# Optimization experiments

Hardware: AMD Instinct MI355X
Metric: run time of the kernel (lower is better)

## Reference

```python
import jax, jax.numpy as jnp
import numpy as np

B, S, D = 4, 512, 2048
N_HEADS, N_KV, HEAD_DIM = 16, 4, 128
N_REP = N_HEADS // N_KV
FFN = 5632
E, TOPK, R = 8, 2, 16
LORA_SCALE = 32.0 / R  # alpha / r
EPS = 1e-5


def setup_inputs() -> dict:
    key = jax.random.key(0)
    ks = jax.random.split(key, 32)

    def p(k, shape, s=0.02):
        return jax.random.normal(k, shape, jnp.float32) * s

    data = jax.random.normal(ks[0], (B, S, D), jnp.float32)
    # causal additive mask [1,1,S,S]
    causal = jnp.tril(jnp.ones((S, S), jnp.bool_))
    mask = jnp.where(causal, 0.0, -1e9).astype(jnp.float32)[None, None]
    # rotary angles (llama interleaved pairing), half head_dim
    inv_freq = 1.0 / (10000.0 ** (np.arange(0, HEAD_DIM, 2, dtype=np.float32) / HEAD_DIM))
    angles = jnp.asarray(np.arange(S, dtype=np.float32)[:, None] * inv_freq[None, :])
    rope_cos = jnp.cos(angles)  # [S, HEAD_DIM//2]
    rope_sin = jnp.sin(angles)

    inp = dict(
        data=data, mask=mask, rope_cos=rope_cos, rope_sin=rope_sin,
        att_norm_w=jnp.ones((D,), jnp.float32),
        ffn_norm_w=jnp.ones((D,), jnp.float32),
        wq=p(ks[1], (D, D)), wk=p(ks[2], (N_KV * HEAD_DIM, D)),
        wv=p(ks[3], (N_KV * HEAD_DIM, D)), wo=p(ks[4], (D, D)),
        lqA=p(ks[5], (R, D)), lqB=p(ks[6], (D, R)),
        lkA=p(ks[7], (R, D)), lkB=p(ks[8], (N_KV * HEAD_DIM, R)),
        lvA=p(ks[9], (R, D)), lvB=p(ks[10], (N_KV * HEAD_DIM, R)),
        loA=p(ks[11], (R, D)), loB=p(ks[12], (D, R)),
        w1=p(ks[13], (FFN, D)), w2=p(ks[14], (D, FFN)), w3=p(ks[15], (FFN, D)),
        gate_w=p(ks[16], (E, D)),
        eA1=p(ks[17], (E, R, D)), eB1=p(ks[18], (E, FFN, R)),
        eA2=p(ks[19], (E, R, FFN)), eB2=p(ks[20], (E, D, R)),
        eA3=p(ks[21], (E, R, D)), eB3=p(ks[22], (E, FFN, R)),
    )
    return inp


def rmsnorm(x, w):
    return x * jax.lax.rsqrt(jnp.mean(x * x, axis=-1, keepdims=True) + EPS) * w


def lora_linear(x, W, A, Bm):
    # torch Linear weight is [out, in]; lora: x @ A^T @ B^T * scale
    return x @ W.T + ((x @ A.T) @ Bm.T) * LORA_SCALE


def apply_rope(x, cos, sin):
    # x: [B,S,H,Dh]; interleaved complex rotation per pair
    x1, x2 = x[..., 0::2], x[..., 1::2]
    c = cos[None, :, None, :]
    s = sin[None, :, None, :]
    o1 = x1 * c - x2 * s
    o2 = x1 * s + x2 * c
    return jnp.stack([o1, o2], axis=-1).reshape(x.shape)


def transformer_fwd(data, mask, rope_cos, rope_sin, att_norm_w, ffn_norm_w,
                    wq, wk, wv, wo, lqA, lqB, lkA, lkB, lvA, lvB, loA, loB,
                    w1, w2, w3, gate_w, eA1, eB1, eA2, eB2, eA3, eB3):
    b, s, _ = data.shape
    h = rmsnorm(data, att_norm_w)
    xq = lora_linear(h, wq, lqA, lqB).reshape(b, s, N_HEADS, HEAD_DIM)
    xk = lora_linear(h, wk, lkA, lkB).reshape(b, s, N_KV, HEAD_DIM)
    xv = lora_linear(h, wv, lvA, lvB).reshape(b, s, N_KV, HEAD_DIM)
    xq = apply_rope(xq, rope_cos, rope_sin)
    xk = apply_rope(xk, rope_cos, rope_sin)
    # repeat_kv: each kv head repeated n_rep times consecutively
    xk = jnp.repeat(xk, N_REP, axis=2)
    xv = jnp.repeat(xv, N_REP, axis=2)
    scores = jnp.einsum('bshd,bthd->bhst', xq, xk) / jnp.sqrt(jnp.float32(HEAD_DIM))
    scores = scores + mask
    attn = jax.nn.softmax(scores, axis=-1)
    out = jnp.einsum('bhst,bthd->bshd', attn, xv).reshape(b, s, D)
    data = data + lora_linear(out, wo, loA, loB)

    # MoE FFN (MixLoRA): shared base w1/w2/w3 + per-expert LoRA, top-k routing
    hn = rmsnorm(data, ffn_norm_w)
    x = hn.reshape(b * s, D)
    logits = x @ gate_w.T                       # [T, E]
    probs = jax.nn.softmax(logits, axis=-1)
    vals, idx = jax.lax.top_k(probs, TOPK)      # [T, k]
    vals = vals / jnp.sum(vals, axis=-1, keepdims=True)
    T = b * s
    route = jnp.zeros((T, E), x.dtype).at[jnp.arange(T)[:, None], idx].set(vals)
    h1 = x @ w1.T   # shared base projections
    h3 = x @ w3.T
    acc = jnp.zeros((T, D), x.dtype)
    for e in range(E):
        g1 = h1 + ((x @ eA1[e].T) @ eB1[e].T) * LORA_SCALE
        g3 = h3 + ((x @ eA3[e].T) @ eB3[e].T) * LORA_SCALE
        gh = jax.nn.silu(g1) * g3
        oe = gh @ w2.T + ((gh @ eA2[e].T) @ eB2[e].T) * LORA_SCALE
        acc = acc + route[:, e:e + 1] * oe
    return data + acc.reshape(b, s, D)


def reference(data, mask, rope_cos, rope_sin, att_norm_w, ffn_norm_w,
              wq, wk, wv, wo, lqA, lqB, lkA, lkB, lvA, lvB, loA, loB,
              w1, w2, w3, gate_w, eA1, eB1, eA2, eB2, eA3, eB3):
    return transformer_fwd(data, mask, rope_cos, rope_sin, att_norm_w, ffn_norm_w,
                           wq, wk, wv, wo, lqA, lqB, lkA, lkB, lvA, lvB, loA, loB,
                           w1, w2, w3, gate_w, eA1, eB1, eA2, eB2, eA3, eB3)
```

## Files before the change

kernel.cpp:

```cpp
#include <hip/hip_runtime.h>
#include <stdint.h>

#define DI static __device__ __forceinline__

typedef __attribute__((ext_vector_type(8))) short bf16x8;
typedef __attribute__((ext_vector_type(4))) float floatx4;

DI unsigned short f2bf(float x){
  unsigned int u = __float_as_uint(x);
  u += 0x7fffu + ((u >> 16) & 1u);
  return (unsigned short)(u >> 16);
}
DI float bf2f(unsigned short h){ return __uint_as_float(((unsigned int)h) << 16); }

#define GLOAD16(gp, lp) \
  __builtin_amdgcn_global_load_lds((const __attribute__((address_space(1))) unsigned int*)(gp), \
                                   (__attribute__((address_space(3))) unsigned int*)(lp), 16, 0, 0)

#define WAITVM(n) asm volatile("s_waitcnt vmcnt(" #n ")" ::: "memory")

template<int OUTM, int RESM, bool CSKIP, bool SPLIT>
__global__ __launch_bounds__(256, 2)
void k_gemm(const unsigned short* __restrict__ A, long lda, long sA1, long sA2, long aLo,
            const unsigned short* __restrict__ B, long ldb, long sB1, long sB2, long bLo,
            void* __restrict__ C, long ldc, long sC1, long sC2, long cLo,
            const void* __restrict__ Rz, long ldr,
            const unsigned short* __restrict__ G1p, const float* __restrict__ ewp, int slot,
            int kIters, int zshift, int bshift)
{
  if (CSKIP && blockIdx.y > blockIdx.x) return;
  __shared__ __attribute__((aligned(16))) unsigned short As[SPLIT ? 8192 : 4096];
  __shared__ __attribute__((aligned(16))) unsigned short Bs[SPLIT ? 8192 : 4096];
  const int tid = threadIdx.x;
  const int w = tid >> 6, lane = tid & 63;
  const int wm = (w >> 1) * 64, wn = (w & 1) * 64;
  const int z = blockIdx.z;
  const int zr = z & ((1 << zshift) - 1);
  const int zb = z >> zshift;
  long k0 = 0;
  if (OUTM == 2 || OUTM == 8) k0 = (long)zb * (long)kIters * 32;
  const unsigned short* Ab = A + (long)((OUTM==8)?0:zb) * sA2 + (long)zr * sA1 + (long)blockIdx.x * 128 * lda + k0;
  const unsigned short* Bb = B + (long)((OUTM==8)?0:zb) * sB2 + (long)(zr >> bshift) * sB1 + (long)blockIdx.y * 128 * ldb + k0;

  const int rlo = w * 16 + (lane & 15);
  const int rhi = 64 + rlo;
  const int cc  = (lane >> 4) * 8;
  unsigned short* ldsA0 = As + w * 512;
  unsigned short* ldsA1 = As + 2048 + w * 512;
  unsigned short* ldsB0 = Bs + w * 512;
  unsigned short* ldsB1 = Bs + 2048 + w * 512;

  floatx4 acc[4][4];
  floatx4 zv = {0.f, 0.f, 0.f, 0.f};
#pragma unroll
  for (int i = 0; i < 4; ++i)
#pragma unroll
    for (int j = 0; j < 4; ++j) acc[i][j] = zv;

  const int abase = (wm >> 4) * 512 + lane * 8;
  const int bbase = (wn >> 4) * 512 + lane * 8;

  for (int kt = 0; kt < kIters; ++kt) {
    const unsigned short* pa = Ab + (long)kt * 32;
    const unsigned short* pb = Bb + (long)kt * 32;
    GLOAD16(pa + (long)rlo * lda + cc, ldsA0);
    GLOAD16(pa + (long)rhi * lda + cc, ldsA1);
    GLOAD16(pb + (long)rlo * ldb + cc, ldsB0);
    GLOAD16(pb + (long)rhi * ldb + cc, ldsB1);
    if (SPLIT) {
      const unsigned short* pal = pa + aLo;
      const unsigned short* pbl = pb + bLo;
      GLOAD16(pal + (long)rlo * lda + cc, As + 4096 + w * 512);
      GLOAD16(pal + (long)rhi * lda + cc, As + 6144 + w * 512);
      GLOAD16(pbl + (long)rlo * ldb + cc, Bs + 4096 + w * 512);
      GLOAD16(pbl + (long)rhi * ldb + cc, Bs + 6144 + w * 512);
    }
    __syncthreads();
    bf16x8 af[4], bfr[4];
#pragma unroll
    for (int i = 0; i < 4; ++i)
      af[i] = *(const bf16x8*)(As + abase + i * 512);
#pragma unroll
    for (int j = 0; j < 4; ++j)
      bfr[j] = *(const bf16x8*)(Bs + bbase + j * 512);
    if (SPLIT) {
      bf16x8 al[4], bl[4];
#pragma unroll
      for (int i = 0; i < 4; ++i)
        al[i] = *(const bf16x8*)(As + 4096 + abase + i * 512);
#pragma unroll
      for (int j = 0; j < 4; ++j)
        bl[j] = *(const bf16x8*)(Bs + 4096 + bbase + j * 512);
#pragma unroll
      for (int i = 0; i < 4; ++i)
#pragma unroll
        for (int j = 0; j < 4; ++j) {
          acc[i][j] = __builtin_amdgcn_mfma_f32_16x16x32_bf16(af[i], bfr[j], acc[i][j], 0, 0, 0);
          acc[i][j] = __builtin_amdgcn_mfma_f32_16x16x32_bf16(af[i], bl[j], acc[i][j], 0, 0, 0);
          acc[i][j] = __builtin_amdgcn_mfma_f32_16x16x32_bf16(al[i], bfr[j], acc[i][j], 0, 0, 0);
        }
    } else {
#pragma unroll
      for (int i = 0; i < 4; ++i)
#pragma unroll
        for (int j = 0; j < 4; ++j)
          acc[i][j] = __builtin_amdgcn_mfma_f32_16x16x32_bf16(af[i], bfr[j], acc[i][j], 0, 0, 0);
    }
    __syncthreads();
  }

  const long mb = (long)blockIdx.x * 128 + wm + ((lane >> 4) * 4);
  const long nb = (long)blockIdx.y * 128 + wn + (lane & 15);
  const long cbase = (long)zb * sC2 + (long)zr * sC1;
#pragma unroll
  for (int i = 0; i < 4; ++i) {
#pragma unroll
    for (int j = 0; j < 4; ++j) {
#pragma unroll
      for (int rr = 0; rr < 4; ++rr) {
        long m = mb + i * 16 + rr;
        long n = nb + j * 16;
        float v = acc[i][j][rr];
        if (RESM == 1) v += ((const float*)Rz)[m * ldr + n];
        if (RESM == 2) v += bf2f(((const unsigned short*)Rz)[m * ldr + n]);
        if (OUTM == 0 || OUTM == 8) ((float*)C)[cbase + m * ldc + n] = v;
        else if (OUTM == 1) ((unsigned short*)C)[cbase + m * ldc + n] = f2bf(v);
        else if (OUTM == 2) atomicAdd((float*)C + cbase + m * ldc + n, v);
        else if (OUTM == 4) {
          float g1 = bf2f(G1p[m * ldc + n]);
          float s1 = g1 / (1.f + __expf(-g1));
          ((unsigned short*)C)[cbase + m * ldc + n] = f2bf(ewp[m * 2 + slot] * s1 * v);
        } else if (OUTM == 5) {
          unsigned short h = f2bf(v);
          unsigned short l = f2bf(v - bf2f(h));
          ((unsigned short*)C)[cbase + m * ldc + n] = h;
          ((unsigned short*)C)[cbase + m * ldc + n + cLo] = l;
        } else {
          long bq = m >> 9, sI = m & 511, kv = n >> 7, dI = n & 127;
          long t = (((bq * 4 + kv) * 128 + dI) << 9) + sI;
          unsigned short h = f2bf(v);
          unsigned short l = f2bf(v - bf2f(h));
          ((unsigned short*)C)[t] = h;
          ((unsigned short*)C)[t + cLo] = l;
        }
      }
    }
  }
}

template<int BM, int BN, bool SPLIT, int OUTM>
__global__ __launch_bounds__(512, 2)
void k_gemm2(const unsigned short* __restrict__ A, long lda, long aLo,
             const unsigned short* __restrict__ B, long ldb, long bLo,
             void* __restrict__ C, long ldc, long sC2, int kIters)
{
  constexpr int DEPTH = 4;
  constexpr int ASZ = BM * 32 * (SPLIT ? 2 : 1);
  constexpr int BSZ = BN * 32 * (SPLIT ? 2 : 1);
  constexpr int TSZ = ASZ + BSZ;
  constexpr int FM = BM / 32, FN = BN / 64;
  constexpr int LPT = (SPLIT ? 2 : 1) * (BM / 128 + BN / 128);
  static_assert(LPT == 3 || LPT == 4, "vmcnt constants assume LPT in {3,4}");
  __shared__ __attribute__((aligned(16))) unsigned short sm[DEPTH * TSZ];

  const int tid = threadIdx.x;
  const int w = tid >> 6, lane = tid & 63;
  const int wm = (w >> 2) * (BM / 2), wn = (w & 3) * (BN / 4);
  const int zb = blockIdx.z;
  const long k0 = (OUTM == 8) ? (long)zb * (long)kIters * 32 : 0;
  const unsigned short* Ab = A + (long)blockIdx.x * BM * lda + k0;
  const unsigned short* Bb = B + (long)blockIdx.y * BN * ldb + k0;
  const int rA = lane & 15;
  const int cc = (lane >> 4) * 8;

  floatx4 acc[FM][FN];
  floatx4 zv = {0.f, 0.f, 0.f, 0.f};
#pragma unroll
  for (int i = 0; i < FM; ++i)
#pragma unroll
    for (int j = 0; j < FN; ++j) acc[i][j] = zv;

  auto stage = [&](int kt) {
    const unsigned short* pa = Ab + (long)kt * 32;
    const unsigned short* pb = Bb + (long)kt * 32;
    unsigned short* sa = sm + (size_t)(kt & (DEPTH - 1)) * TSZ;
    unsigned short* sb = sa + ASZ;
#pragma unroll
    for (int r = 0; r < BM / 128; ++r) {
      const int b = r * 8 + w;
      const long row = b * 16 + rA;
      GLOAD16(pa + row * lda + cc, sa + b * 512);
      if (SPLIT) GLOAD16(pa + aLo + row * lda + cc, sa + BM * 32 + b * 512);
    }
#pragma unroll
    for (int r = 0; r < BN / 128; ++r) {
      const int b = r * 8 + w;
      const long row = b * 16 + rA;
      GLOAD16(pb + row * ldb + cc, sb + b * 512);
      if (SPLIT) GLOAD16(pb + bLo + row * ldb + cc, sb + BN * 32 + b * 512);
    }
  };

  auto waitpipe = [&](int ahead) {
    if (LPT == 4) {
      if (ahead >= 2) { WAITVM(8); }
      else if (ahead == 1) { WAITVM(4); }
      else { WAITVM(0); }
    } else {
      if (ahead >= 2) { WAITVM(6); }
      else if (ahead == 1) { WAITVM(3); }
      else { WAITVM(0); }
    }
  };

  {
    int np = DEPTH - 1; if (np > kIters) np = kIters;
    for (int p = 0; p < np; ++p) stage(p);
    __builtin_amdgcn_sched_barrier(0);
    waitpipe(np - 1);
    __builtin_amdgcn_s_barrier();
  }

  const int aoff = (wm >> 4) * 512 + lane * 8;
  const int boff = (wn >> 4) * 512 + lane * 8;

  for (int kt = 0; kt < kIters; ++kt) {
    if (kt + DEPTH - 1 < kIters) stage(kt + DEPTH - 1);

    const unsigned short* sa = sm + (size_t)(kt & (DEPTH - 1)) * TSZ;
    const unsigned short* sb = sa + ASZ;
    bf16x8 af[FM], bfr[FN];
#pragma unroll
    for (int i = 0; i < FM; ++i)
      af[i] = *(const bf16x8*)(sa + aoff + i * 512);
#pragma unroll
    for (int j = 0; j < FN; ++j)
      bfr[j] = *(const bf16x8*)(sb + boff + j * 512);
    if (SPLIT) {
      bf16x8 al[FM], bl[FN];
#pragma unroll
      for (int i = 0; i < FM; ++i)
        al[i] = *(const bf16x8*)(sa + BM * 32 + aoff + i * 512);
#pragma unroll
      for (int j = 0; j < FN; ++j)
        bl[j] = *(const bf16x8*)(sb + BN * 32 + boff + j * 512);
      __builtin_amdgcn_s_setprio(1);
#pragma unroll
      for (int i = 0; i < FM; ++i)
#pragma unroll
        for (int j = 0; j < FN; ++j) {
          acc[i][j] = __builtin_amdgcn_mfma_f32_16x16x32_bf16(af[i], bfr[j], acc[i][j], 0, 0, 0);
          acc[i][j] = __builtin_amdgcn_mfma_f32_16x16x32_bf16(af[i], bl[j], acc[i][j], 0, 0, 0);
          acc[i][j] = __builtin_amdgcn_mfma_f32_16x16x32_bf16(al[i], bfr[j], acc[i][j], 0, 0, 0);
        }
      __builtin_amdgcn_s_setprio(0);
    } else {
      __builtin_amdgcn_s_setprio(1);
#pragma unroll
      for (int i = 0; i < FM; ++i)
#pragma unroll
        for (int j = 0; j < FN; ++j)
          acc[i][j] = __builtin_amdgcn_mfma_f32_16x16x32_bf16(af[i], bfr[j], acc[i][j], 0, 0, 0);
      __builtin_amdgcn_s_setprio(0);
    }

    __builtin_amdgcn_sched_barrier(0);
    int ahead = kIters - 2 - kt;
    if (ahead > DEPTH - 2) ahead = DEPTH - 2;
    if (ahead < 0) ahead = 0;
    waitpipe(ahead);
    __builtin_amdgcn_s_barrier();
  }

  const long mb = (long)blockIdx.x * BM + wm + ((lane >> 4) * 4);
  const long nb = (long)blockIdx.y * BN + wn + (lane & 15);
  const long cbase = (long)zb * sC2;
#pragma unroll
  for (int i = 0; i < FM; ++i) {
#pragma unroll
    for (int j = 0; j < FN; ++j) {
#pragma unroll
      for (int rr = 0; rr < 4; ++rr) {
        long m = mb + i * 16 + rr;
        long n = nb + j * 16;
        float v = acc[i][j][rr];
        if (OUTM == 8) ((float*)C)[cbase + m * ldc + n] = v;
        else ((unsigned short*)C)[m * ldc + n] = f2bf(v);
      }
    }
  }
}

__global__ void k_rmsnorm(const float* __restrict__ x, const float* __restrict__ w,
                          unsigned short* __restrict__ ob, long loOff){
  int t = blockIdx.x;
  const float* row = x + (size_t)t * 2048;
  float ss = 0.f;
  for (int i = threadIdx.x; i < 2048; i += 256){ float v = row[i]; ss += v * v; }
#pragma unroll
  for (int o = 32; o; o >>= 1) ss += __shfl_xor(ss, o);
  __shared__ float sred[4]; __shared__ float srms;
  int lane = threadIdx.x & 63, wid = threadIdx.x >> 6;
  if (lane == 0) sred[wid] = ss;
  __syncthreads();
  if (threadIdx.x == 0) srms = rsqrtf((sred[0]+sred[1]+sred[2]+sred[3]) * (1.f/2048.f) + 1e-5f);
  __syncthreads();
  float rr = srms;
  for (int i = threadIdx.x; i < 2048; i += 256){
    float v = row[i] * rr * w[i];
    unsigned short h = f2bf(v);
    ob[(size_t)t * 2048 + i] = h;
    if (loOff) ob[(size_t)t * 2048 + i + loOff] = f2bf(v - bf2f(h));
  }
}

__global__ void k_fold(const float* __restrict__ W, const float* __restrict__ Bm,
                       const float* __restrict__ A, unsigned short* __restrict__ out, long loOff){
  int idx = blockIdx.x * 256 + threadIdx.x;
  int n = idx >> 11, k = idx & 2047;
  float acc = W[idx];
  const float* br = Bm + (size_t)n * 16;
#pragma unroll
  for (int r = 0; r < 16; ++r) acc += 2.0f * br[r] * A[r * 2048 + k];
  unsigned short h = f2bf(acc);
  out[idx] = h;
  out[idx + loOff] = f2bf(acc - bf2f(h));
}

__global__ void k_cvt4(const float* __restrict__ in, unsigned short* __restrict__ out){
  int i = (blockIdx.x * 256 + threadIdx.x) * 4;
  float4 v = *(const float4*)(in + i);
  unsigned long long pk = (unsigned long long)f2bf(v.x)
    | ((unsigned long long)f2bf(v.y) << 16)
    | ((unsigned long long)f2bf(v.z) << 32)
    | ((unsigned long long)f2bf(v.w) << 48);
  *(unsigned long long*)(out + i) = pk;
}

__global__ void k_beff(const float* __restrict__ eB, unsigned short* __restrict__ out, int F){
  int idx = blockIdx.x * 256 + threadIdx.x;
  int f = idx >> 7, er = idx & 127;
  int e = er >> 4, r = er & 15;
  out[idx] = f2bf(eB[((size_t)e * F + f) * 16 + r]);
}

__global__ void k_qkv_epi(const float* __restrict__ P,
                          const float* __restrict__ rc, const float* __restrict__ rs,
                          unsigned short* __restrict__ qb, unsigned short* __restrict__ kb,
                          unsigned short* __restrict__ vT){
  int idx = blockIdx.x * 256 + threadIdx.x;
  int t = idx / 1536, p = idx - t * 1536;
  int c = p * 2;
  const float2 a = *(const float2*)(P + (size_t)t * 3072 + c);
  const float2 b = *(const float2*)(P + 6291456 + (size_t)t * 3072 + c);
  float v0 = a.x + b.x, v1 = a.y + b.y;
  int s = t & 511;
  if (c < 2560) {
    int i = (c & 127) >> 1;
    float co = rc[s * 64 + i], sn = rs[s * 64 + i];
    float o0 = v0 * co - v1 * sn;
    float o1 = v0 * sn + v1 * co;
    v0 = o0; v1 = o1;
  }
  unsigned short h0 = f2bf(v0), l0 = f2bf(v0 - bf2f(h0));
  unsigned short h1 = f2bf(v1), l1 = f2bf(v1 - bf2f(h1));
  if (c < 2048) {
    size_t o = (size_t)t * 2048 + c;
    qb[o] = h0; qb[o + 1] = h1;
    qb[o + 4194304] = l0; qb[o + 4194305] = l1;
  } else if (c < 2560) {
    size_t o = (size_t)t * 512 + (c - 2048);
    kb[o] = h0; kb[o + 1] = h1;
    kb[o + 1048576] = l0; kb[o + 1048577] = l1;
  } else {
    int d = c - 2560;
    int kv = d >> 7, dI = d & 127, bq = t >> 9;
    size_t o = (((size_t)(bq * 4 + kv) * 128 + dI) << 9) + s;
    vT[o] = h0; vT[o + 512] = h1;
    vT[o + 1048576] = l0; vT[o + 1048576 + 512] = l1;
  }
}

__global__ void k_add2res(const float* __restrict__ P, const float* __restrict__ res,
                          float* __restrict__ out){
  int i = (blockIdx.x * 256 + threadIdx.x) * 4;
  float4 a = *(const float4*)(P + i);
  float4 b = *(const float4*)(P + 4194304 + i);
  float4 r = *(const float4*)(res + i);
  float4 o; o.x = a.x + b.x + r.x; o.y = a.y + b.y + r.y;
  o.z = a.z + b.z + r.z; o.w = a.w + b.w + r.w;
  *(float4*)(out + i) = o;
}

__global__ void k_softmax(float* __restrict__ sp){
  int row = blockIdx.x;
  int s = row & 511;
  float* in = sp + (size_t)row * 512;
  unsigned short* op = (unsigned short*)in;
  int t0 = threadIdx.x, t1 = threadIdx.x + 256;
  const float scale = 0.088388347648318447f;
  float v0 = (t0 <= s) ? in[t0] * scale : -3.0e38f;
  float v1 = (t1 <= s) ? in[t1] * scale : -3.0e38f;
  float mx = fmaxf(v0, v1);
#pragma unroll
  for (int o = 32; o; o >>= 1) mx = fmaxf(mx, __shfl_xor(mx, o));
  __shared__ float sred[8];
  int lane = threadIdx.x & 63, wid = threadIdx.x >> 6;
  if (lane == 0) sred[wid] = mx;
  __syncthreads();
  mx = fmaxf(fmaxf(sred[0], sred[1]), fmaxf(sred[2], sred[3]));
  float e0 = (t0 <= s) ? __expf(v0 - mx) : 0.f;
  float e1 = (t1 <= s) ? __expf(v1 - mx) : 0.f;
  float sum = e0 + e1;
#pragma unroll
  for (int o = 32; o; o >>= 1) sum += __shfl_xor(sum, o);
  if (lane == 0) sred[4 + wid] = sum;
  __syncthreads();
  sum = sred[4] + sred[5] + sred[6] + sred[7];
  float inv = 1.f / sum;
  float p0 = e0 * inv, p1 = e1 * inv;
  unsigned short h0 = f2bf(p0), h1 = f2bf(p1);
  op[t0] = h0; op[512 + t0] = f2bf(p0 - bf2f(h0));
  op[t1] = h1; op[512 + t1] = f2bf(p1 - bf2f(h1));
}

__global__ void k_route(const float* __restrict__ x2, const float* __restrict__ w,
                        const float* __restrict__ gw, int* __restrict__ eidx,
                        float* __restrict__ ew){
  int t = blockIdx.x; int lane = threadIdx.x;
  const float* row = x2 + (size_t)t * 2048;
  float ss = 0.f;
  for (int d = lane; d < 2048; d += 64){ float v = row[d]; ss += v * v; }
#pragma unroll
  for (int o = 32; o; o >>= 1) ss += __shfl_xor(ss, o);
  float rr = rsqrtf(ss * (1.f/2048.f) + 1e-5f);
  float acc[8] = {0,0,0,0,0,0,0,0};
  for (int d = lane; d < 2048; d += 64){
    float xv = row[d] * rr * w[d];
#pragma unroll
    for (int e = 0; e < 8; ++e) acc[e] += xv * gw[e * 2048 + d];
  }
#pragma unroll
  for (int e = 0; e < 8; ++e)
#pragma unroll
    for (int o = 32; o; o >>= 1) acc[e] += __shfl_xor(acc[e], o);
  if (lane == 0){
    int i0 = 0;
#pragma unroll
    for (int e = 1; e < 8; ++e) if (acc[e] > acc[i0]) i0 = e;
    int i1 = -1;
#pragma unroll
    for (int e = 0; e < 8; ++e) if (e != i0 && (i1 < 0 || acc[e] > acc[i1])) i1 = e;
    float p1 = __expf(acc[i1] - acc[i0]);
    float inv = 1.f / (1.f + p1);
    eidx[t * 2 + 0] = i0; eidx[t * 2 + 1] = i1;
    ew[t * 2 + 0] = inv;  ew[t * 2 + 1] = p1 * inv;
  }
}

__global__ void k_zero(float* __restrict__ p){
  p[(size_t)blockIdx.x * 256 + threadIdx.x] = 0.f;
}

__global__ void k_ubuild(const float* __restrict__ U1, const float* __restrict__ U3,
                         const int* __restrict__ eidx,
                         unsigned short* __restrict__ u10, unsigned short* __restrict__ u11,
                         unsigned short* __restrict__ u30, unsigned short* __restrict__ u31){
  int idx = blockIdx.x * 256 + threadIdx.x;
  int t = idx >> 7, j = idx & 127; int e = j >> 4;
  int e0 = eidx[t * 2], e1 = eidx[t * 2 + 1];
  float v1 = U1[idx] * 2.0f, v3 = U3[idx] * 2.0f;
  u10[idx] = (e == e0) ? f2bf(v1) : (unsigned short)0;
  u11[idx] = (e == e1) ? f2bf(v1) : (unsigned short)0;
  u30[idx] = (e == e0) ? f2bf(v3) : (unsigned short)0;
  u31[idx] = (e == e1) ? f2bf(v3) : (unsigned short)0;
}

__global__ void k_addip(unsigned short* __restrict__ a, const unsigned short* __restrict__ b){
  size_t i = (size_t)blockIdx.x * 256 + threadIdx.x;
  a[i] = f2bf(bf2f(a[i]) + bf2f(b[i]));
}

__global__ void k_vhat(const float* __restrict__ U20, const float* __restrict__ U21,
                       const int* __restrict__ eidx, unsigned short* __restrict__ out){
  int idx = blockIdx.x * 256 + threadIdx.x;
  int t = idx >> 7, j = idx & 127; int e = j >> 4;
  int e0 = eidx[t * 2], e1 = eidx[t * 2 + 1];
  float v = 0.f;
  if (e == e0) v = 2.0f * U20[idx];
  else if (e == e1) v = 2.0f * U21[idx];
  out[idx] = f2bf(v);
}

extern "C" void kernel_launch(void* const* d_in, const int* in_sizes, int n_in,
                              void* d_out, int out_size, void* d_ws, size_t ws_size,
                              hipStream_t stream){
  const float* data  = (const float*)d_in[0];
  const float* rcos  = (const float*)d_in[2];
  const float* rsin  = (const float*)d_in[3];
  const float* attw  = (const float*)d_in[4];
  const float* ffnw  = (const float*)d_in[5];
  const float* wq    = (const float*)d_in[6];
  const float* wk    = (const float*)d_in[7];
  const float* wv    = (const float*)d_in[8];
  const float* wo    = (const float*)d_in[9];
  const float* lqA   = (const float*)d_in[10];
  const float* lqB   = (const float*)d_in[11];
  const float* lkA   = (const float*)d_in[12];
  const float* lkB   = (const float*)d_in[13];
  const float* lvA   = (const float*)d_in[14];
  const float* lvB   = (const float*)d_in[15];
  const float* loA   = (const float*)d_in[16];
  const float* loB   = (const float*)d_in[17];
  const float* w1    = (const float*)d_in[18];
  const float* w2    = (const float*)d_in[19];
  const float* w3    = (const float*)d_in[20];
  const float* gatew = (const float*)d_in[21];
  const float* eA1   = (const float*)d_in[22];
  const float* eB1   = (const float*)d_in[23];
  const float* eA2   = (const float*)d_in[24];
  const float* eB2   = (const float*)d_in[25];
  const float* eA3   = (const float*)d_in[26];
  const float* eB3   = (const float*)d_in[27];
  (void)in_sizes; (void)n_in; (void)out_size; (void)ws_size;

  char* base = (char*)d_ws;
  float* data2 = (float*)d_out;

  unsigned short* hb   = (unsigned short*)(base + 0);
  unsigned short* Wqkv = (unsigned short*)(base + 16777216);
  float*          QKVf = (float*)(base + 41943040);
  unsigned short* qb   = (unsigned short*)(base + 92274688);
  unsigned short* kb   = (unsigned short*)(base + 109051904);
  unsigned short* vT   = (unsigned short*)(base + 113246208);
  float*          sc   = (float*)(base + 0);
  unsigned short* scU  = (unsigned short*)(base + 0);
  unsigned short* ao   = (unsigned short*)(base + 67108864);
  unsigned short* Wo   = (unsigned short*)(base + 0);
  float*          Wof  = (float*)(base + 16777216);

  size_t off = 0;
  auto alloc = [&](size_t n)->char*{ char* p = base + off; off = (off + n + 255) & ~(size_t)255; return p; };
  int*   eidx = (int*)alloc(16384);
  float* ew   = (float*)alloc(16384);
  unsigned short* hnb  = (unsigned short*)alloc(8388608);
  unsigned short* h1b  = (unsigned short*)alloc(23068672);
  unsigned short* h3b  = (unsigned short*)alloc(23068672);
  unsigned short* wbuf = (unsigned short*)alloc(23068672);
  unsigned short* gh0  = (unsigned short*)alloc(23068672);
  unsigned short* eA1c = (unsigned short*)alloc(524288);
  unsigned short* eA3c = (unsigned short*)alloc(524288);
  unsigned short* eA2c = (unsigned short*)alloc(1441792);
  unsigned short* Bf1  = (unsigned short*)alloc(1441792);
  unsigned short* Bf3  = (unsigned short*)alloc(1441792);
  unsigned short* Bf2  = (unsigned short*)alloc(524288);
  float* Uz = (float*)alloc(4194304);
  float* U1 = Uz, *U3 = Uz + 262144, *U20 = Uz + 524288, *U21 = Uz + 786432;
  unsigned short* Ut10 = (unsigned short*)alloc(524288);
  unsigned short* Ut11 = (unsigned short*)alloc(524288);
  unsigned short* Ut30 = (unsigned short*)alloc(524288);
  unsigned short* Ut31 = (unsigned short*)alloc(524288);
  unsigned short* vhat = (unsigned short*)alloc(524288);
  unsigned short* gh1  = h1b;
  float*          W2f  = (float*)h1b;

  k_rmsnorm<<<2048, 256, 0, stream>>>(data, attw, hb, 4194304);
  k_fold<<<16384, 256, 0, stream>>>(wq, lqB, lqA, Wqkv, 6291456);
  k_fold<<<4096, 256, 0, stream>>>(wk, lkB, lkA, Wqkv + 4194304, 6291456);
  k_fold<<<4096, 256, 0, stream>>>(wv, lvB, lvA, Wqkv + 5242880, 6291456);

  k_gemm2<128,128,true,8><<<dim3(16,24,2), 512, 0, stream>>>(
      hb, 2048, 4194304, Wqkv, 2048, 6291456, QKVf, 3072, 6291456, 32);
  k_qkv_epi<<<12288, 256, 0, stream>>>(QKVf, rcos, rsin, qb, kb, vT);

  k_gemm<0,0,true,true><<<dim3(4,4,64), 256, 0, stream>>>(
      qb, 2048, 128, 1048576, 4194304, kb, 512, 128, 262144, 1048576,
      sc, 512, 262144, 4194304, 0, nullptr,0, nullptr,nullptr,0, 4, 4, 2);
  k_softmax<<<32768, 256, 0, stream>>>(sc);
  k_gemm<5,0,false,true><<<dim3(4,1,64), 256, 0, stream>>>(
      scU, 1024, 524288, 8388608, 512, vT, 512, 65536, 262144, 1048576,
      ao, 2048, 128, 1048576, 4194304, nullptr,0, nullptr,nullptr,0, 16, 4, 2);

  k_fold<<<16384, 256, 0, stream>>>(wo, loB, loA, Wo, 4194304);
  k_gemm2<128,128,true,8><<<dim3(16,16,2), 512, 0, stream>>>(
      ao, 2048, 4194304, Wo, 2048, 4194304, Wof, 2048, 4194304, 32);
  k_add2res<<<4096, 256, 0, stream>>>(Wof, data, data2);

  k_rmsnorm<<<2048, 256, 0, stream>>>(data2, ffnw, hnb, 0);
  k_route<<<2048, 64, 0, stream>>>(data2, ffnw, gatew, eidx, ew);

  k_cvt4<<<11264, 256, 0, stream>>>(w1, wbuf);
  k_gemm2<256,256,false,1><<<dim3(8,22,1), 512, 0, stream>>>(
      hnb, 2048, 0, wbuf, 2048, 0, h1b, 5632, 0, 64);
  k_cvt4<<<11264, 256, 0, stream>>>(w3, wbuf);
  k_gemm2<256,256,false,1><<<dim3(8,22,1), 512, 0, stream>>>(
      hnb, 2048, 0, wbuf, 2048, 0, h3b, 5632, 0, 64);

  k_cvt4<<<256, 256, 0, stream>>>(eA1, eA1c);
  k_cvt4<<<256, 256, 0, stream>>>(eA3, eA3c);
  k_cvt4<<<704, 256, 0, stream>>>(eA2, eA2c);
  k_beff<<<2816, 256, 0, stream>>>(eB1, Bf1, 5632);
  k_beff<<<2816, 256, 0, stream>>>(eB3, Bf3, 5632);
  k_beff<<<1024, 256, 0, stream>>>(eB2, Bf2, 2048);
  k_zero<<<4096, 256, 0, stream>>>(Uz);

  k_gemm<2,0,false,false><<<dim3(16,1,8), 256, 0, stream>>>(
      hnb,2048,0,0,0, eA1c,2048,0,0,0, U1,128,0,0,0, nullptr,0, nullptr,nullptr,0, 8,0,0);
  k_gemm<2,0,false,false><<<dim3(16,1,8), 256, 0, stream>>>(
      hnb,2048,0,0,0, eA3c,2048,0,0,0, U3,128,0,0,0, nullptr,0, nullptr,nullptr,0, 8,0,0);
  k_ubuild<<<1024, 256, 0, stream>>>(U1, U3, eidx, Ut10, Ut11, Ut30, Ut31);

  k_gemm<1,2,false,false><<<dim3(16,44,1), 256, 0, stream>>>(
      Ut10,128,0,0,0, Bf1,128,0,0,0, wbuf,5632,0,0,0, h1b,5632, nullptr,nullptr,0, 4,0,0);
  k_gemm<4,2,false,false><<<dim3(16,44,1), 256, 0, stream>>>(
      Ut30,128,0,0,0, Bf3,128,0,0,0, gh0,5632,0,0,0, h3b,5632, wbuf,ew,0, 4,0,0);
  k_gemm<2,0,false,false><<<dim3(16,1,8), 256, 0, stream>>>(
      gh0,5632,0,0,0, eA2c,5632,0,0,0, U20,128,0,0,0, nullptr,0, nullptr,nullptr,0, 22,0,0);
  k_gemm<1,2,false,false><<<dim3(16,44,1), 256, 0, stream>>>(
      Ut11,128,0,0,0, Bf1,128,0,0,0, wbuf,5632,0,0,0, h1b,5632, nullptr,nullptr,0, 4,0,0);
  k_gemm<4,2,false,false><<<dim3(16,44,1), 256, 0, stream>>>(
      Ut31,128,0,0,0, Bf3,128,0,0,0, gh1,5632,0,0,0, h3b,5632, wbuf,ew,1, 4,0,0);
  k_gemm<2,0,false,false><<<dim3(16,1,8), 256, 0, stream>>>(
      gh1,5632,0,0,0, eA2c,5632,0,0,0, U21,128,0,0,0, nullptr,0, nullptr,nullptr,0, 22,0,0);

  k_addip<<<45056, 256, 0, stream>>>(gh0, gh1);
  k_vhat<<<1024, 256, 0, stream>>>(U20, U21, eidx, vhat);
  k_gemm<2,0,false,false><<<dim3(16,16,1), 256, 0, stream>>>(
      vhat,128,0,0,0, Bf2,128,0,0,0, data2,2048,0,0,0, nullptr,0, nullptr,nullptr,0, 4,0,0);
  k_cvt4<<<11264, 256, 0, stream>>>(w2, wbuf);
  k_gemm2<128,256,false,8><<<dim3(16,8,2), 512, 0, stream>>>(
      gh0, 5632, 0, wbuf, 5632, 0, W2f, 2048, 4194304, 88);
  k_add2res<<<4096, 256, 0, stream>>>(W2f, data2, data2);
}
```

Baseline: 1.058 ms.

## Parametrize gemm2 pipeline depth and shrink tiles; port LoRA-expand GEMMs to gemm2

Makes the k_gemm2 pipeline depth a template parameter and runs every gemm2 launch at depth 2 with 128x128 tiles, replacing the 256x256 tiles on the FFN w1/w3 GEMMs and the 128x256 tile on the w2 GEMM. Residual-add and SiLU-gating epilogues are added to gemm2 so the four expert LoRA-B expansion GEMMs move from the older k_gemm to gemm2. The goal is more blocks for occupancy and less shared memory per block. In exchange, the depth-2 pipeline waits for all loads every iteration, which exposes more memory latency, and the smaller tiles give less data reuse.

Result: slower. 1.129 ms (+6.8%).

```diff
diff --git a/kernel.cpp b/kernel.cpp
--- a/kernel.cpp
+++ b/kernel.cpp
@@ -148,19 +148,21 @@
   }
 }
 
-template<int BM, int BN, bool SPLIT, int OUTM>
+template<int BM, int BN, bool SPLIT, int OUTM, int RESM, int DEPTH>
 __global__ __launch_bounds__(512, 2)
 void k_gemm2(const unsigned short* __restrict__ A, long lda, long aLo,
              const unsigned short* __restrict__ B, long ldb, long bLo,
-             void* __restrict__ C, long ldc, long sC2, int kIters)
+             void* __restrict__ C, long ldc, long sC2,
+             const void* __restrict__ Rz, long ldr,
+             const unsigned short* __restrict__ G1p, const float* __restrict__ ewp, int slot,
+             int kIters)
 {
-  constexpr int DEPTH = 4;
   constexpr int ASZ = BM * 32 * (SPLIT ? 2 : 1);
   constexpr int BSZ = BN * 32 * (SPLIT ? 2 : 1);
   constexpr int TSZ = ASZ + BSZ;
   constexpr int FM = BM / 32, FN = BN / 64;
   constexpr int LPT = (SPLIT ? 2 : 1) * (BM / 128 + BN / 128);
-  static_assert(LPT == 3 || LPT == 4, "vmcnt constants assume LPT in {3,4}");
+  static_assert(LPT >= 2 && LPT <= 4, "vmcnt constants assume LPT in {2,3,4}");
   __shared__ __attribute__((aligned(16))) unsigned short sm[DEPTH * TSZ];
 
   const int tid = threadIdx.x;
@@ -202,13 +204,18 @@
   };
 
   auto waitpipe = [&](int ahead) {
+    if (DEPTH == 2) { WAITVM(0); return; }
     if (LPT == 4) {
       if (ahead >= 2) { WAITVM(8); }
       else if (ahead == 1) { WAITVM(4); }
       else { WAITVM(0); }
-    } else {
+    } else if (LPT == 3) {
       if (ahead >= 2) { WAITVM(6); }
       else if (ahead == 1) { WAITVM(3); }
+      else { WAITVM(0); }
+    } else {
+      if (ahead >= 2) { WAITVM(4); }
+      else if (ahead == 1) { WAITVM(2); }
       else { WAITVM(0); }
     }
   };
@@ -284,7 +291,13 @@
         long m = mb + i * 16 + rr;
         long n = nb + j * 16;
         float v = acc[i][j][rr];
+        if (RESM == 2) v += bf2f(((const unsigned short*)Rz)[m * ldr + n]);
         if (OUTM == 8) ((float*)C)[cbase + m * ldc + n] = v;
+        else if (OUTM == 4) {
+          float g1 = bf2f(G1p[m * ldc + n]);
+          float s1 = g1 / (1.f + __expf(-g1));
+          ((unsigned short*)C)[m * ldc + n] = f2bf(ewp[m * 2 + slot] * s1 * v);
+        }
         else ((unsigned short*)C)[m * ldc + n] = f2bf(v);
       }
     }
@@ -569,8 +582,9 @@
   k_fold<<<4096, 256, 0, stream>>>(wk, lkB, lkA, Wqkv + 4194304, 6291456);
   k_fold<<<4096, 256, 0, stream>>>(wv, lvB, lvA, Wqkv + 5242880, 6291456);
 
-  k_gemm2<128,128,true,8><<<dim3(16,24,2), 512, 0, stream>>>(
-      hb, 2048, 4194304, Wqkv, 2048, 6291456, QKVf, 3072, 6291456, 32);
+  k_gemm2<128,128,true,8,0,2><<<dim3(16,24,2), 512, 0, stream>>>(
+      hb, 2048, 4194304, Wqkv, 2048, 6291456, QKVf, 3072, 6291456,
+      nullptr, 0, nullptr, nullptr, 0, 32);
   k_qkv_epi<<<12288, 256, 0, stream>>>(QKVf, rcos, rsin, qb, kb, vT);
 
   k_gemm<0,0,true,true><<<dim3(4,4,64), 256, 0, stream>>>(
@@ -582,19 +596,22 @@
       ao, 2048, 128, 1048576, 4194304, nullptr,0, nullptr,nullptr,0, 16, 4, 2);
 
   k_fold<<<16384, 256, 0, stream>>>(wo, loB, loA, Wo, 4194304);
-  k_gemm2<128,128,true,8><<<dim3(16,16,2), 512, 0, stream>>>(
-      ao, 2048, 4194304, Wo, 2048, 4194304, Wof, 2048, 4194304, 32);
+  k_gemm2<128,128,true,8,0,2><<<dim3(16,16,2), 512, 0, stream>>>(
+      ao, 2048, 4194304, Wo, 2048, 4194304, Wof, 2048, 4194304,
+      nullptr, 0, nullptr, nullptr, 0, 32);
   k_add2res<<<4096, 256, 0, stream>>>(Wof, data, data2);
 
   k_rmsnorm<<<2048, 256, 0, stream>>>(data2, ffnw, hnb, 0);
   k_route<<<2048, 64, 0, stream>>>(data2, ffnw, gatew, eidx, ew);
 
   k_cvt4<<<11264, 256, 0, stream>>>(w1, wbuf);
-  k_gemm2<256,256,false,1><<<dim3(8,22,1), 512, 0, stream>>>(
-      hnb, 2048, 0, wbuf, 2048, 0, h1b, 5632, 0, 64);
+  k_gemm2<128,128,false,1,0,2><<<dim3(16,44,1), 512, 0, stream>>>(
+      hnb, 2048, 0, wbuf, 2048, 0, h1b, 5632, 0,
+      nullptr, 0, nullptr, nullptr, 0, 64);
   k_cvt4<<<11264, 256, 0, stream>>>(w3, wbuf);
-  k_gemm2<256,256,false,1><<<dim3(8,22,1), 512, 0, stream>>>(
-      hnb, 2048, 0, wbuf, 2048, 0, h3b, 5632, 0, 64);
+  k_gemm2<128,128,false,1,0,2><<<dim3(16,44,1), 512, 0, stream>>>(
+      hnb, 2048, 0, wbuf, 2048, 0, h3b, 5632, 0,
+      nullptr, 0, nullptr, nullptr, 0, 64);
 
   k_cvt4<<<256, 256, 0, stream>>>(eA1, eA1c);
   k_cvt4<<<256, 256, 0, stream>>>(eA3, eA3c);
@@ -610,16 +627,20 @@
       hnb,2048,0,0,0, eA3c,2048,0,0,0, U3,128,0,0,0, nullptr,0, nullptr,nullptr,0, 8,0,0);
   k_ubuild<<<1024, 256, 0, stream>>>(U1, U3, eidx, Ut10, Ut11, Ut30, Ut31);
 
-  k_gemm<1,2,false,false><<<dim3(16,44,1), 256, 0, stream>>>(
-      Ut10,128,0,0,0, Bf1,128,0,0,0, wbuf,5632,0,0,0, h1b,5632, nullptr,nullptr,0, 4,0,0);
-  k_gemm<4,2,false,false><<<dim3(16,44,1), 256, 0, stream>>>(
-      Ut30,128,0,0,0, Bf3,128,0,0,0, gh0,5632,0,0,0, h3b,5632, wbuf,ew,0, 4,0,0);
+  k_gemm2<128,128,false,1,2,2><<<dim3(16,44,1), 512, 0, stream>>>(
+      Ut10, 128, 0, Bf1, 128, 0, wbuf, 5632, 0,
+      h1b, 5632, nullptr, nullptr, 0, 4);
+  k_gemm2<128,128,false,4,2,2><<<dim3(16,44,1), 512, 0, stream>>>(
+      Ut30, 128, 0, Bf3, 128, 0, gh0, 5632, 0,
+      h3b, 5632, wbuf, ew, 0, 4);
   k_gemm<2,0,false,false><<<dim3(16,1,8), 256, 0, stream>>>(
       gh0,5632,0,0,0, eA2c,5632,0,0,0, U20,128,0,0,0, nullptr,0, nullptr,nullptr,0, 22,0,0);
-  k_gemm<1,2,false,false><<<dim3(16,44,1), 256, 0, stream>>>(
-      Ut11,128,0,0,0, Bf1,128,0,0,0, wbuf,5632,0,0,0, h1b,5632, nullptr,nullptr,0, 4,0,0);
-  k_gemm<4,2,false,false><<<dim3(16,44,1), 256, 0, stream>>>(
-      Ut31,128,0,0,0, Bf3,128,0,0,0, gh1,5632,0,0,0, h3b,5632, wbuf,ew,1, 4,0,0);
+  k_gemm2<128,128,false,1,2,2><<<dim3(16,44,1), 512, 0, stream>>>(
+      Ut11, 128, 0, Bf1, 128, 0, wbuf, 5632, 0,
+      h1b, 5632, nullptr, nullptr, 0, 4);
+  k_gemm2<128,128,false,4,2,2><<<dim3(16,44,1), 512, 0, stream>>>(
+      Ut31, 128, 0, Bf3, 128, 0, gh1, 5632, 0,
+      h3b, 5632, wbuf, ew, 1, 4);
   k_gemm<2,0,false,false><<<dim3(16,1,8), 256, 0, stream>>>(
       gh1,5632,0,0,0, eA2c,5632,0,0,0, U21,128,0,0,0, nullptr,0, nullptr,nullptr,0, 22,0,0);
 
@@ -628,7 +649,8 @@
   k_gemm<2,0,false,false><<<dim3(16,16,1), 256, 0, stream>>>(
       vhat,128,0,0,0, Bf2,128,0,0,0, data2,2048,0,0,0, nullptr,0, nullptr,nullptr,0, 4,0,0);
   k_cvt4<<<11264, 256, 0, stream>>>(w2, wbuf);
-  k_gemm2<128,256,false,8><<<dim3(16,8,2), 512, 0, stream>>>(
-      gh0, 5632, 0, wbuf, 5632, 0, W2f, 2048, 4194304, 88);
+  k_gemm2<128,128,false,8,0,2><<<dim3(16,16,2), 512, 0, stream>>>(
+      gh0, 5632, 0, wbuf, 5632, 0, W2f, 2048, 4194304,
+      nullptr, 0, nullptr, nullptr, 0, 88);
   k_add2res<<<4096, 256, 0, stream>>>(W2f, data2, data2);
 }
```

## Switch gemm2 to double-buffered pipeline with larger tiles and per-row A fragment loads

Applied to the files above, without the earlier changes.

Makes the pipeline depth of k_gemm2 a template parameter and sets it to 2 everywhere. The loop now prefetches one stage ahead and waits with vmcnt(0) each iteration. The QKV and Wo projections move to larger 256-wide tiles with fewer blocks. A fragments are now loaded per row inside the MFMA loop rather than all up front, lowering register pressure. The intent is to free shared memory for the larger tiles and raise per-block data reuse, at the cost of less latency hiding and fewer blocks for the smaller GEMMs.

New measurement: 1.084 ms. 2.5% more time.

```diff
diff --git a/kernel.cpp b/kernel.cpp
--- a/kernel.cpp
+++ b/kernel.cpp
@@ -17,7 +17,7 @@
   __builtin_amdgcn_global_load_lds((const __attribute__((address_space(1))) unsigned int*)(gp), \
                                    (__attribute__((address_space(3))) unsigned int*)(lp), 16, 0, 0)
 
-#define WAITVM(n) asm volatile("s_waitcnt vmcnt(" #n ")" ::: "memory")
+#define WAITVM0 asm volatile("s_waitcnt vmcnt(0)" ::: "memory")
 
 template<int OUTM, int RESM, bool CSKIP, bool SPLIT>
 __global__ __launch_bounds__(256, 2)
@@ -148,19 +148,16 @@
   }
 }
 
-template<int BM, int BN, bool SPLIT, int OUTM>
+template<int BM, int BN, bool SPLIT, int OUTM, int DEPTH>
 __global__ __launch_bounds__(512, 2)
 void k_gemm2(const unsigned short* __restrict__ A, long lda, long aLo,
              const unsigned short* __restrict__ B, long ldb, long bLo,
              void* __restrict__ C, long ldc, long sC2, int kIters)
 {
-  constexpr int DEPTH = 4;
   constexpr int ASZ = BM * 32 * (SPLIT ? 2 : 1);
   constexpr int BSZ = BN * 32 * (SPLIT ? 2 : 1);
   constexpr int TSZ = ASZ + BSZ;
   constexpr int FM = BM / 32, FN = BN / 64;
-  constexpr int LPT = (SPLIT ? 2 : 1) * (BM / 128 + BN / 128);
-  static_assert(LPT == 3 || LPT == 4, "vmcnt constants assume LPT in {3,4}");
   __shared__ __attribute__((aligned(16))) unsigned short sm[DEPTH * TSZ];
 
   const int tid = threadIdx.x;
@@ -201,74 +198,57 @@
     }
   };
 
-  auto waitpipe = [&](int ahead) {
-    if (LPT == 4) {
-      if (ahead >= 2) { WAITVM(8); }
-      else if (ahead == 1) { WAITVM(4); }
-      else { WAITVM(0); }
-    } else {
-      if (ahead >= 2) { WAITVM(6); }
-      else if (ahead == 1) { WAITVM(3); }
-      else { WAITVM(0); }
-    }
-  };
-
-  {
-    int np = DEPTH - 1; if (np > kIters) np = kIters;
-    for (int p = 0; p < np; ++p) stage(p);
-    __builtin_amdgcn_sched_barrier(0);
-    waitpipe(np - 1);
-    __builtin_amdgcn_s_barrier();
-  }
+  stage(0);
+  __builtin_amdgcn_sched_barrier(0);
+  WAITVM0;
+  __builtin_amdgcn_s_barrier();
 
   const int aoff = (wm >> 4) * 512 + lane * 8;
   const int boff = (wn >> 4) * 512 + lane * 8;
 
   for (int kt = 0; kt < kIters; ++kt) {
-    if (kt + DEPTH - 1 < kIters) stage(kt + DEPTH - 1);
+    if (kt + 1 < kIters) stage(kt + 1);
 
     const unsigned short* sa = sm + (size_t)(kt & (DEPTH - 1)) * TSZ;
     const unsigned short* sb = sa + ASZ;
-    bf16x8 af[FM], bfr[FN];
-#pragma unroll
-    for (int i = 0; i < FM; ++i)
-      af[i] = *(const bf16x8*)(sa + aoff + i * 512);
-#pragma unroll
-    for (int j = 0; j < FN; ++j)
-      bfr[j] = *(const bf16x8*)(sb + boff + j * 512);
     if (SPLIT) {
-      bf16x8 al[FM], bl[FN];
-#pragma unroll
-      for (int i = 0; i < FM; ++i)
-        al[i] = *(const bf16x8*)(sa + BM * 32 + aoff + i * 512);
-#pragma unroll
-      for (int j = 0; j < FN; ++j)
-        bl[j] = *(const bf16x8*)(sb + BN * 32 + boff + j * 512);
+      bf16x8 bfr[FN], bl[FN];
+#pragma unroll
+      for (int j = 0; j < FN; ++j) {
+        bfr[j] = *(const bf16x8*)(sb + boff + j * 512);
+        bl[j]  = *(const bf16x8*)(sb + BN * 32 + boff + j * 512);
+      }
       __builtin_amdgcn_s_setprio(1);
 #pragma unroll
-      for (int i = 0; i < FM; ++i)
+      for (int i = 0; i < FM; ++i) {
+        bf16x8 ai = *(const bf16x8*)(sa + aoff + i * 512);
+        bf16x8 ali = *(const bf16x8*)(sa + BM * 32 + aoff + i * 512);
 #pragma unroll
         for (int j = 0; j < FN; ++j) {
-          acc[i][j] = __builtin_amdgcn_mfma_f32_16x16x32_bf16(af[i], bfr[j], acc[i][j], 0, 0, 0);
-          acc[i][j] = __builtin_amdgcn_mfma_f32_16x16x32_bf16(af[i], bl[j], acc[i][j], 0, 0, 0);
-          acc[i][j] = __builtin_amdgcn_mfma_f32_16x16x32_bf16(al[i], bfr[j], acc[i][j], 0, 0, 0);
+          acc[i][j] = __builtin_amdgcn_mfma_f32_16x16x32_bf16(ai, bfr[j], acc[i][j], 0, 0, 0);
+          acc[i][j] = __builtin_amdgcn_mfma_f32_16x16x32_bf16(ai, bl[j], acc[i][j], 0, 0, 0);
+          acc[i][j] = __builtin_amdgcn_mfma_f32_16x16x32_bf16(ali, bfr[j], acc[i][j], 0, 0, 0);
         }
+      }
       __builtin_amdgcn_s_setprio(0);
     } else {
+      bf16x8 bfr[FN];
+#pragma unroll
+      for (int j = 0; j < FN; ++j)
+        bfr[j] = *(const bf16x8*)(sb + boff + j * 512);
       __builtin_amdgcn_s_setprio(1);
 #pragma unroll
-      for (int i = 0; i < FM; ++i)
+      for (int i = 0; i < FM; ++i) {
+        bf16x8 ai = *(const bf16x8*)(sa + aoff + i * 512);
 #pragma unroll
         for (int j = 0; j < FN; ++j)
-          acc[i][j] = __builtin_amdgcn_mfma_f32_16x16x32_bf16(af[i], bfr[j], acc[i][j], 0, 0, 0);
+          acc[i][j] = __builtin_amdgcn_mfma_f32_16x16x32_bf16(ai, bfr[j], acc[i][j], 0, 0, 0);
+      }
       __builtin_amdgcn_s_setprio(0);
     }
 
     __builtin_amdgcn_sched_barrier(0);
-    int ahead = kIters - 2 - kt;
-    if (ahead > DEPTH - 2) ahead = DEPTH - 2;
-    if (ahead < 0) ahead = 0;
-    waitpipe(ahead);
+    WAITVM0;
     __builtin_amdgcn_s_barrier();
   }
 
@@ -569,7 +549,7 @@
   k_fold<<<4096, 256, 0, stream>>>(wk, lkB, lkA, Wqkv + 4194304, 6291456);
   k_fold<<<4096, 256, 0, stream>>>(wv, lvB, lvA, Wqkv + 5242880, 6291456);
 
-  k_gemm2<128,128,true,8><<<dim3(16,24,2), 512, 0, stream>>>(
+  k_gemm2<256,256,true,8,2><<<dim3(8,12,2), 512, 0, stream>>>(
       hb, 2048, 4194304, Wqkv, 2048, 6291456, QKVf, 3072, 6291456, 32);
   k_qkv_epi<<<12288, 256, 0, stream>>>(QKVf, rcos, rsin, qb, kb, vT);
 
@@ -582,7 +562,7 @@
       ao, 2048, 128, 1048576, 4194304, nullptr,0, nullptr,nullptr,0, 16, 4, 2);
 
   k_fold<<<16384, 256, 0, stream>>>(wo, loB, loA, Wo, 4194304);
-  k_gemm2<128,128,true,8><<<dim3(16,16,2), 512, 0, stream>>>(
+  k_gemm2<256,128,true,8,2><<<dim3(8,16,2), 512, 0, stream>>>(
       ao, 2048, 4194304, Wo, 2048, 4194304, Wof, 2048, 4194304, 32);
   k_add2res<<<4096, 256, 0, stream>>>(Wof, data, data2);
 
@@ -590,10 +570,10 @@
   k_route<<<2048, 64, 0, stream>>>(data2, ffnw, gatew, eidx, ew);
 
   k_cvt4<<<11264, 256, 0, stream>>>(w1, wbuf);
-  k_gemm2<256,256,false,1><<<dim3(8,22,1), 512, 0, stream>>>(
+  k_gemm2<256,256,false,1,2><<<dim3(8,22,1), 512, 0, stream>>>(
       hnb, 2048, 0, wbuf, 2048, 0, h1b, 5632, 0, 64);
   k_cvt4<<<11264, 256, 0, stream>>>(w3, wbuf);
-  k_gemm2<256,256,false,1><<<dim3(8,22,1), 512, 0, stream>>>(
+  k_gemm2<256,256,false,1,2><<<dim3(8,22,1), 512, 0, stream>>>(
       hnb, 2048, 0, wbuf, 2048, 0, h3b, 5632, 0, 64);
 
   k_cvt4<<<256, 256, 0, stream>>>(eA1, eA1c);
@@ -628,7 +608,7 @@
   k_gemm<2,0,false,false><<<dim3(16,16,1), 256, 0, stream>>>(
       vhat,128,0,0,0, Bf2,128,0,0,0, data2,2048,0,0,0, nullptr,0, nullptr,nullptr,0, 4,0,0);
   k_cvt4<<<11264, 256, 0, stream>>>(w2, wbuf);
-  k_gemm2<128,256,false,8><<<dim3(16,8,2), 512, 0, stream>>>(
+  k_gemm2<128,256,false,8,2><<<dim3(16,8,2), 512, 0, stream>>>(
       gh0, 5632, 0, wbuf, 5632, 0, W2f, 2048, 4194304, 88);
   k_add2res<<<4096, 256, 0, stream>>>(W2f, data2, data2);
 }
```
